# Optimization experiments

Measured on AMD Instinct MI355X. Metric: run time of the kernel, lower is better.

## Reference

```python
import jax, jax.numpy as jnp
import numpy as np

N = 13627
E = 504378
D = 500


def _seg_softmax(e, seg, n):
    m = jax.ops.segment_max(e, seg, num_segments=n)
    ex = jnp.exp(e - m[seg])
    s = jax.ops.segment_sum(ex, seg, num_segments=n)
    return ex / (s[seg] + 1e-16)


def _gatv2(x, src, dst, Wl, Wr, att, b, n):
    # PyG GATv2Conv (heads=1): message = Wl x_src; score uses Wl x_src + Wr x_dst
    xl = x @ Wl                                   # [N, F]
    xr = x @ Wr                                   # [N, F]
    e = jax.nn.leaky_relu(xl[src] + xr[dst], 0.2) @ att   # [E]
    a = _seg_softmax(e, dst, n)                   # segment softmax over targets
    out = jax.ops.segment_sum(a[:, None] * xl[src], dst, num_segments=n)
    return out + b


def setup_inputs() -> dict:
    key = jax.random.key(0)
    ks = jax.random.split(key, 24)
    s = 0.05
    inp = {
        'x': jax.random.normal(ks[0], (N, D), dtype=jnp.float32),
        'edge_index': jax.random.randint(ks[1], (2, E), 0, N),
        'neg_edge_index': jax.random.randint(ks[2], (2, E), 0, N),
        'Wl1': jax.random.normal(ks[3], (D, 300)) * s,
        'Wr1': jax.random.normal(ks[4], (D, 300)) * s,
        'att1': jax.random.normal(ks[5], (300,)) * s,
        'b1': jnp.zeros((300,)),
        'Wl2': jax.random.normal(ks[6], (300, 100)) * s,
        'Wr2': jax.random.normal(ks[7], (300, 100)) * s,
        'att2': jax.random.normal(ks[8], (100,)) * s,
        'b2': jnp.zeros((100,)),
        'Wl3': jax.random.normal(ks[9], (100, 1)) * s,
        'Wr3': jax.random.normal(ks[10], (100, 1)) * s,
        'att3': jax.random.normal(ks[11], (1,)) * s,
        'b3': jnp.zeros((1,)),
        'W_lin1': jax.random.normal(ks[12], (D, 100)) * s,
        'b_lin1': jnp.zeros((100,)),
        'W_lin2': jax.random.normal(ks[13], (D, 100)) * s,
        'b_lin2': jnp.zeros((100,)),
        'c1': jnp.array([0.5], dtype=jnp.float32),
        'c2': jnp.array([0.5], dtype=jnp.float32),
    }
    return inp


def reference(x, edge_index, neg_edge_index, Wl1, Wr1, att1, b1, Wl2, Wr2, att2, b2,
              Wl3, Wr3, att3, b3, W_lin1, b_lin1, W_lin2, b_lin2, c1, c2):
    # eval mode: dropout / dropout_adj are identity
    loops = jnp.arange(N)
    src = jnp.concatenate([edge_index[0], loops])   # GATv2Conv adds self loops
    dst = jnp.concatenate([edge_index[1], loops])

    h1 = jax.nn.relu(_gatv2(x, src, dst, Wl1, Wr1, att1, b1, N))
    h2 = jax.nn.relu(_gatv2(h1, src, dst, Wl2, Wr2, att2, b2, N))

    xo = h2 + jax.nn.relu(x @ W_lin1 + b_lin1)
    z = h2 + jax.nn.relu(x @ W_lin2 + b_lin2)

    # link-prediction reconstruction loss
    pos_s = jnp.sum(z[edge_index[0]] * z[edge_index[1]], axis=1)
    pos_loss = -jnp.mean(jnp.log(jax.nn.sigmoid(pos_s) + 1e-15))
    neg_s = jnp.sum(z[neg_edge_index[0]] * z[neg_edge_index[1]], axis=1)
    neg_loss = -jnp.mean(jnp.log(1.0 - jax.nn.sigmoid(neg_s) + 1e-15))
    r_loss = pos_loss + neg_loss

    out = _gatv2(xo, src, dst, Wl3, Wr3, att3, b3, N)   # [N, 1]
    return out, r_loss, c1, c2
```

## Files before the change

### kernel.cpp

```cpp
#include <hip/hip_runtime.h>
#include <hip/hip_bf16.h>

#define NODES 13627
#define DIM   500

typedef short short8 __attribute__((ext_vector_type(8)));
typedef float f32x4 __attribute__((ext_vector_type(4)));
typedef float floatx2 __attribute__((ext_vector_type(2)));

__device__ inline float wave_reduce_sum(float v) {
#pragma unroll
    for (int o = 32; o > 0; o >>= 1) v += __shfl_xor(v, o, 64);
    return v;
}

__device__ inline void store_v(float* p, float v) { *p = v; }
__device__ inline void store_v(__hip_bfloat16* p, float v) { *p = __float2bfloat16(v); }

__device__ inline float blo(unsigned w) { unsigned t = w << 16;        return __builtin_bit_cast(float, t); }
__device__ inline float bhi(unsigned w) { unsigned t = w & 0xffff0000u; return __builtin_bit_cast(float, t); }

__device__ inline unsigned char to_fp8(float v) {
    int r = __builtin_amdgcn_cvt_pk_fp8_f32(v, v, 0, false);
    return (unsigned char)(r & 0xff);
}

__device__ inline unsigned pk2bf(float a, float b) {
    unsigned la = (unsigned)__builtin_bit_cast(unsigned short, __float2bfloat16(a));
    unsigned hb = (unsigned)__builtin_bit_cast(unsigned short, __float2bfloat16(b));
    return la | (hb << 16);
}

template <int CTRL>
__device__ inline float dpp_add_step(float v) {
    int s = __builtin_amdgcn_update_dpp(0, __builtin_bit_cast(int, v), CTRL, 0xf, 0xf, true);
    return v + __builtin_bit_cast(float, s);
}
__device__ inline float quad16_reduce(float v) {
    v = dpp_add_step<0x128>(v);
    v = dpp_add_step<0x124>(v);
    v = dpp_add_step<0x4E>(v);
    v = dpp_add_step<0xB1>(v);
    return v;
}

struct b4 { __hip_bfloat16 a, b, c, d; };

__global__ __launch_bounds__(256) void hist_kernel(const int* __restrict__ dst,
                                                   int* __restrict__ cnt, int E) {
    int i = blockIdx.x * blockDim.x + threadIdx.x;
    if (i < E) atomicAdd(&cnt[dst[i]], 1);
}

__global__ __launch_bounds__(1024) void scan_kernel(int* __restrict__ cnt_cur,
                                                    int* __restrict__ off, int n) {
    __shared__ int wsum[16];
    const int tid = threadIdx.x, lane = tid & 63, w = tid >> 6;
    int carry = 0;
    for (int base = 0; base < n; base += 1024) {
        int i = base + tid;
        int v = (i < n) ? cnt_cur[i] : 0;
        int s = v;
#pragma unroll
        for (int o = 1; o < 64; o <<= 1) {
            int t = __shfl_up(s, o, 64);
            if (lane >= o) s += t;
        }
        if (lane == 63) wsum[w] = s;
        __syncthreads();
        if (w == 0 && lane < 16) {
            int x = wsum[lane];
            int sx = x;
#pragma unroll
            for (int o = 1; o < 16; o <<= 1) {
                int t = __shfl_up(sx, o, 64);
                if (lane >= o) sx += t;
            }
            wsum[lane] = sx;
        }
        __syncthreads();
        int wo = (w == 0) ? 0 : wsum[w - 1];
        int total = wsum[15];
        int excl = carry + wo + (s - v);
        if (i < n) { off[i] = excl; cnt_cur[i] = excl; }
        carry += total;
        __syncthreads();
    }
    if (tid == 0) off[n] = carry;
}

__global__ __launch_bounds__(256) void scatter_kernel(const int* __restrict__ src,
                                                      const int* __restrict__ dst,
                                                      int* __restrict__ cur,
                                                      int* __restrict__ ssrc, int E) {
    int i = blockIdx.x * blockDim.x + threadIdx.x;
    if (i < E) {
        int p = atomicAdd(&cur[dst[i]], 1);
        ssrc[p] = src[i];
    }
}

__global__ __launch_bounds__(256) void convert_all_kernel(
    const float* __restrict__ x,
    const float* __restrict__ Wl1, const float* __restrict__ Wr1,
    const float* __restrict__ Wl2, const float* __restrict__ Wr2,
    const float* __restrict__ Ws1, const float* __restrict__ Ws2,
    const float* __restrict__ bs1, const float* __restrict__ bs2,
    __hip_bfloat16* __restrict__ W1T, __hip_bfloat16* __restrict__ W2T,
    __hip_bfloat16* __restrict__ WsT, float* __restrict__ bcat,
    __hip_bfloat16* __restrict__ xb, int M) {
    int i = blockIdx.x * 256 + threadIdx.x;
    if (i < 327680) {
        int n = i >> 9, k = i & 511;
        float v = 0.f;
        if (k < 500) {
            if (n < 300) v = Wl1[k * 300 + n];
            else if (n < 600) v = Wr1[k * 300 + n - 300];
        }
        W1T[i] = __float2bfloat16(v);
    } else if (i < 409600) {
        int j = i - 327680;
        int n = j / 320, k = j - n * 320;
        float v = 0.f;
        if (k < 300) {
            if (n < 100) v = Wl2[k * 100 + n];
            else if (n < 200) v = Wr2[k * 100 + n - 100];
        }
        W2T[j] = __float2bfloat16(v);
    } else if (i < 540672) {
        int j = i - 409600;
        int n = j >> 9, k = j & 511;
        float v = 0.f;
        if (k < 500) {
            if (n < 100) v = Ws1[k * 100 + n];
            else if (n < 200) v = Ws2[k * 100 + n - 100];
        }
        WsT[j] = __float2bfloat16(v);
    } else if (i < 540928) {
        int n = i - 540672;
        float v = 0.f;
        if (n < 100) v = bs1[n];
        else if (n < 200) v = bs2[n - 100];
        bcat[n] = v;
    } else {
        int j = i - 540928;
        if (j >= M * 128) return;
        int m = j >> 7, k = (j & 127) << 2;
        b4 o;
        if (k < 500) {
            float4 v = *(const float4*)(x + (size_t)m * 500 + k);
            o.a = __float2bfloat16(v.x); o.b = __float2bfloat16(v.y);
            o.c = __float2bfloat16(v.z); o.d = __float2bfloat16(v.w);
        } else {
            o.a = o.b = o.c = o.d = __float2bfloat16(0.f);
        }
        *(b4*)(xb + (size_t)m * 512 + k) = o;
    }
}

template <int EPI, typename TC>
__global__ __launch_bounds__(256) void mfma_gemm(
    const __hip_bfloat16* __restrict__ A, const __hip_bfloat16* __restrict__ BT,
    TC* __restrict__ C, const float* __restrict__ bias, const float* __restrict__ h2,
    unsigned char* __restrict__ p8, __hip_bfloat16* __restrict__ pb,
    int M, int Kp, int Nn, int ldc) {
    __shared__ short AsF[8 * 64 * 8];
    __shared__ short BsF[4 * 64 * 8];
    const int t = threadIdx.x;
    const int w = t >> 6, lane = t & 63;
    const int c = t & 3, rr = t >> 2;
    const int m0 = blockIdx.y * 128, n0 = blockIdx.x * 64;

    f32x4 acc[2][4];
#pragma unroll
    for (int i = 0; i < 2; i++)
#pragma unroll
        for (int j = 0; j < 4; j++) acc[i][j] = (f32x4){0.f, 0.f, 0.f, 0.f};

    for (int k0 = 0; k0 < Kp; k0 += 32) {
#pragma unroll
        for (int r = 0; r < 2; r++) {
            int m = r * 64 + rr;
            int gm = m0 + m; if (gm >= M) gm = M - 1;
            float4 v = *(const float4*)(A + (size_t)gm * Kp + k0 + c * 8);
            int mi = m >> 4, sl = m & 15;
            *(float4*)(&AsF[(mi * 64 + c * 16 + sl) * 8]) = v;
        }
        {
            int n = rr;
            float4 v = *(const float4*)(BT + (size_t)(n0 + n) * Kp + k0 + c * 8);
            int ni = n >> 4, sl = n & 15;
            *(float4*)(&BsF[(ni * 64 + c * 16 + sl) * 8]) = v;
        }
        __syncthreads();
        short8 a0 = *(const short8*)(&AsF[((w * 2 + 0) * 64 + lane) * 8]);
        short8 a1 = *(const short8*)(&AsF[((w * 2 + 1) * 64 + lane) * 8]);
#pragma unroll
        for (int j = 0; j < 4; j++) {
            short8 b = *(const short8*)(&BsF[(j * 64 + lane) * 8]);
            acc[0][j] = __builtin_amdgcn_mfma_f32_16x16x32_bf16(a0, b, acc[0][j], 0, 0, 0);
            acc[1][j] = __builtin_amdgcn_mfma_f32_16x16x32_bf16(a1, b, acc[1][j], 0, 0, 0);
        }
        __syncthreads();
    }

    const int q = lane >> 4, sl = lane & 15;
#pragma unroll
    for (int i = 0; i < 2; i++) {
#pragma unroll
        for (int j = 0; j < 4; j++) {
#pragma unroll
            for (int reg = 0; reg < 4; reg++) {
                int gm = m0 + w * 32 + i * 16 + q * 4 + reg;
                int gn = n0 + j * 16 + sl;
                if (gm >= M) continue;
                float v = acc[i][j][reg];
                if constexpr (EPI == 1) {
                    if (gn < 300)       p8[(size_t)gm * 304 + gn] = to_fp8(v);
                    else if (gn < 600)  pb[(size_t)gm * 320 + (gn - 300)] = __float2bfloat16(v);
                    else if (gn < 620)  pb[(size_t)gm * 320 + (gn - 300)] = __float2bfloat16(0.f);
                    else if (gn < 624)  p8[(size_t)gm * 304 + (gn - 320)] = 0;
                } else if constexpr (EPI == 2) {
                    if (gn < 100)       p8[(size_t)gm * 112 + gn] = to_fp8(v);
                    else if (gn < 200)  pb[(size_t)gm * 128 + (gn - 100)] = __float2bfloat16(v);
                    else if (gn < 212)  p8[(size_t)gm * 112 + (gn - 100)] = 0;
                    else if (gn < 240)  pb[(size_t)gm * 128 + (gn - 112)] = __float2bfloat16(0.f);
                } else if constexpr (EPI == 3) {
                    if (gn < 200) {
                        int cn = gn < 100 ? gn : gn - 100;
                        float val = fmaxf(v + bias[gn], 0.f) + h2[(size_t)gm * 100 + cn];
                        if (gn < 100) C[(size_t)gm * 100 + gn] = val;
                        else p8[(size_t)gm * 128 + (gn - 100)] = to_fp8(val);
                    } else if (gn < 228) {
                        p8[(size_t)gm * 128 + (gn - 100)] = 0;
                    }
                } else {
                    store_v(&C[(size_t)gm * ldc + gn], v);
                }
            }
        }
    }
}

template <int F, int NJ, int SL8, int SRB, int SOUT, int JSL, typename TOUT>
__global__ __launch_bounds__(64, 4) void gat_f8_kernel(
    const unsigned char* __restrict__ xl8, const __hip_bfloat16* __restrict__ xrb,
    const float* __restrict__ att, const float* __restrict__ bias,
    const int* __restrict__ off, const int* __restrict__ ssrc,
    TOUT* __restrict__ out, int n) {
    const int lane = threadIdx.x;
    const int sl = lane & 15, q = lane >> 4;
    const int wid = blockIdx.x;

    floatx2 attv[NJ * 2], xrv[NJ * 2], acc[NJ * 2];
    const unsigned* xru = (const unsigned*)xrb + (size_t)wid * (SRB / 2);
#pragma unroll
    for (int j = 0; j < NJ; j++) {
        const int f0 = sl * 4 + j * 64;
        if (f0 < F) {
            float4 a4 = *(const float4*)(att + f0);
            attv[j * 2 + 0] = (floatx2){a4.x, a4.y};
            attv[j * 2 + 1] = (floatx2){a4.z, a4.w};
        } else {
            attv[j * 2 + 0] = (floatx2){0.f, 0.f};
            attv[j * 2 + 1] = (floatx2){0.f, 0.f};
        }
        unsigned u0 = __builtin_nontemporal_load(xru + (f0 >> 1));
        unsigned u1 = __builtin_nontemporal_load(xru + (f0 >> 1) + 1);
        xrv[j * 2 + 0] = (floatx2){blo(u0), bhi(u0)};
        xrv[j * 2 + 1] = (floatx2){blo(u1), bhi(u1)};
        acc[j * 2 + 0] = (floatx2){0.f, 0.f};
        acc[j * 2 + 1] = (floatx2){0.f, 0.f};
    }

    const int s0 = off[wid], s1 = off[wid + 1];
    const int eb = s0 - 1;
    const int ee = s1;
    float den = 0.f;
    const int myoff = sl * 4;

    int srcB;
    unsigned u[NJ];
    {
        int eq0 = eb + q;
        int srcA = wid;
        if (eq0 >= s0 && eq0 < ee) srcA = __builtin_nontemporal_load(ssrc + eq0);
        int eq1 = eb + 4 + q;
        srcB = wid;
        if (eq1 >= s0 && eq1 < ee) srcB = __builtin_nontemporal_load(ssrc + eq1);
        const unsigned char* row = xl8 + (size_t)srcA * SL8;
#pragma unroll
        for (int j = 0; j < NJ; j++) {
            const bool ld = (j < NJ - 1) || (sl < JSL);
            u[j] = ld ? *(const unsigned*)(row + myoff + j * 64) : 0u;
        }
    }

    float p_pend = 0.f, gate = 0.f;
    unsigned u_pend[NJ];
#pragma unroll
    for (int j = 0; j < NJ; j++) u_pend[j] = 0u;

    for (int e0 = eb; e0 < ee; e0 += 4) {
        int srcC = wid;
        {
            int eq2 = e0 + 8 + q;
            if (eq2 >= s0 && eq2 < ee) srcC = __builtin_nontemporal_load(ssrc + eq2);
        }
        unsigned un[NJ];
        {
            const unsigned char* row1 = xl8 + (size_t)srcB * SL8;
#pragma unroll
            for (int j = 0; j < NJ; j++) {
                const bool ld = (j < NJ - 1) || (sl < JSL);
                un[j] = ld ? *(const unsigned*)(row1 + myoff + j * 64) : 0u;
            }
        }
        {
            float pp = quad16_reduce(p_pend);
            float ex = gate * __expf(pp);
            den += ex;
            floatx2 ex2 = (floatx2){ex, ex};
#pragma unroll
            for (int j = 0; j < NJ; j++) {
                floatx2 lo = __builtin_amdgcn_cvt_pk_f32_fp8((int)u_pend[j], false);
                floatx2 hi = __builtin_amdgcn_cvt_pk_f32_fp8((int)u_pend[j], true);
                acc[j * 2 + 0] += ex2 * lo;
                acc[j * 2 + 1] += ex2 * hi;
            }
        }
        {
            floatx2 p2 = (floatx2){0.f, 0.f};
#pragma unroll
            for (int j = 0; j < NJ; j++) {
                floatx2 lo = __builtin_amdgcn_cvt_pk_f32_fp8((int)u[j], false);
                floatx2 hi = __builtin_amdgcn_cvt_pk_f32_fp8((int)u[j], true);
                floatx2 s0v = lo + xrv[j * 2 + 0];
                floatx2 s1v = hi + xrv[j * 2 + 1];
                floatx2 g0 = __builtin_elementwise_max(s0v, 0.2f * s0v);
                floatx2 g1 = __builtin_elementwise_max(s1v, 0.2f * s1v);
                p2 += attv[j * 2 + 0] * g0;
                p2 += attv[j * 2 + 1] * g1;
            }
            p_pend = p2.x + p2.y;
            gate = ((e0 + q) < ee) ? 1.f : 0.f;
        }
#pragma unroll
        for (int j = 0; j < NJ; j++) { u_pend[j] = u[j]; u[j] = un[j]; }
        srcB = srcC;
    }
    {
        float pp = quad16_reduce(p_pend);
        float ex = gate * __expf(pp);
        den += ex;
        floatx2 ex2 = (floatx2){ex, ex};
#pragma unroll
        for (int j = 0; j < NJ; j++) {
            floatx2 lo = __builtin_amdgcn_cvt_pk_f32_fp8((int)u_pend[j], false);
            floatx2 hi = __builtin_amdgcn_cvt_pk_f32_fp8((int)u_pend[j], true);
            acc[j * 2 + 0] += ex2 * lo;
            acc[j * 2 + 1] += ex2 * hi;
        }
    }

    float* af = (float*)acc;
#pragma unroll
    for (int o = 16; o <= 32; o <<= 1) {
        den += __shfl_xor(den, o, 64);
#pragma unroll
        for (int i = 0; i < NJ * 4; i++) af[i] += __shfl_xor(af[i], o, 64);
    }

    if (q == 0) {
        const float inv = 1.f / (den + 1e-16f);
#pragma unroll
        for (int j = 0; j < NJ; j++) {
            const int f0 = sl * 4 + j * 64;
            if (f0 >= SOUT) continue;
            float r[4];
#pragma unroll
            for (int cc = 0; cc < 4; cc++) {
                const int f = f0 + cc;
                float v = 0.f;
                if (f < F) v = fmaxf(af[j * 4 + cc] * inv + bias[f], 0.f);
                r[cc] = v;
            }
            if constexpr (sizeof(TOUT) == 4) {
                *(float4*)((float*)out + (size_t)wid * SOUT + f0) =
                    make_float4(r[0], r[1], r[2], r[3]);
            } else {
                unsigned* op = (unsigned*)out + (size_t)wid * (SOUT / 2) + (f0 >> 1);
                op[0] = pk2bf(r[0], r[1]);
                op[1] = pk2bf(r[2], r[3]);
            }
        }
    }
}

__global__ __launch_bounds__(256) void gemm_vec1_kernel(
    const float* __restrict__ xo, const float* __restrict__ wl,
    const float* __restrict__ wr, float* __restrict__ xl3,
    float* __restrict__ xr3, int M, int ldx) {
    const int wid = blockIdx.x * 4 + (threadIdx.x >> 6);
    const int lane = threadIdx.x & 63;
    if (wid >= M) return;
    float a = 0.f, b = 0.f;
    for (int f = lane; f < 100; f += 64) {
        float v = xo[(size_t)wid * ldx + f];
        a += v * wl[f];
        b += v * wr[f];
    }
    a = wave_reduce_sum(a);
    b = wave_reduce_sum(b);
    if (lane == 0) { xl3[wid] = a; xr3[wid] = b; }
}

__global__ __launch_bounds__(256) void gat3_kernel(
    const float* __restrict__ xl3, const float* __restrict__ xr3,
    const float* __restrict__ att3, const float* __restrict__ b3,
    const int* __restrict__ off, const int* __restrict__ ssrc,
    float* __restrict__ out, int n) {
    const int wid = blockIdx.x * 4 + (threadIdx.x >> 6);
    const int lane = threadIdx.x & 63;
    if (wid >= n) return;
    const float xrv = xr3[wid];
    const float att = att3[0];
    float num = 0.f, den = 0.f;
    const int s0 = off[wid], s1 = off[wid + 1];
    for (int e = s0 - 1 + lane; e < s1; e += 64) {
        int src = (e < s0) ? wid : ssrc[e];
        float xlv = xl3[src];
        float t = xlv + xrv;
        float g = t > 0.f ? t : 0.2f * t;
        float ex = __expf(g * att);
        den += ex;
        num += ex * xlv;
    }
    num = wave_reduce_sum(num);
    den = wave_reduce_sum(den);
    if (lane == 0) out[wid] = num / (den + 1e-16f) + b3[0];
}

__global__ __launch_bounds__(256) void loss_kernel(
    const unsigned char* __restrict__ z8, const int* __restrict__ pos,
    const int* __restrict__ neg, float* __restrict__ part, int nb, int E) {
    const int lane = threadIdx.x & 63;
    const int sl = lane & 15;
    const int wlocal = threadIdx.x >> 6;
    const int q = lane >> 4;
    const int nq = gridDim.x * 16;
    const int qid = (blockIdx.x * 4 + wlocal) * 4 + q;
    const int total = 2 * E;
    float psum = 0.f, nsum = 0.f;

    for (int base = qid; base < total; base += 4 * nq) {
        uint2 au[4], bu[4];
        bool act[4], isN[4];
#pragma unroll
        for (int s = 0; s < 4; s++) {
            int it = base + s * nq;
            act[s] = it < total;
            int itc = act[s] ? it : 0;
            isN[s] = itc >= E;
            int e = isN[s] ? itc - E : itc;
            const int* ei = isN[s] ? neg : pos;
            int u = ei[e], v = ei[E + e];
            au[s] = *(const uint2*)(z8 + (size_t)u * 128 + sl * 8);
            bu[s] = *(const uint2*)(z8 + (size_t)v * 128 + sl * 8);
        }
#pragma unroll
        for (int s = 0; s < 4; s++) {
            floatx2 a0 = __builtin_amdgcn_cvt_pk_f32_fp8((int)au[s].x, false);
            floatx2 a1 = __builtin_amdgcn_cvt_pk_f32_fp8((int)au[s].x, true);
            floatx2 a2 = __builtin_amdgcn_cvt_pk_f32_fp8((int)au[s].y, false);
            floatx2 a3 = __builtin_amdgcn_cvt_pk_f32_fp8((int)au[s].y, true);
            floatx2 b0 = __builtin_amdgcn_cvt_pk_f32_fp8((int)bu[s].x, false);
            floatx2 b1 = __builtin_amdgcn_cvt_pk_f32_fp8((int)bu[s].x, true);
            floatx2 b2 = __builtin_amdgcn_cvt_pk_f32_fp8((int)bu[s].y, false);
            floatx2 b3 = __builtin_amdgcn_cvt_pk_f32_fp8((int)bu[s].y, true);
            float p = a0.x * b0.x + a0.y * b0.y + a1.x * b1.x + a1.y * b1.y
                    + a2.x * b2.x + a2.y * b2.y + a3.x * b3.x + a3.y * b3.y;
            p = quad16_reduce(p);
            if (sl == 0 && act[s]) {
                float sig = __builtin_amdgcn_rcpf(1.f + __expf(-p));
                if (isN[s]) nsum += __logf(1.f - sig + 1e-15f);
                else        psum += __logf(sig + 1e-15f);
            }
        }
    }
    float pw = wave_reduce_sum(psum);
    float nw = wave_reduce_sum(nsum);
    __shared__ float sp[4], sn[4];
    if (lane == 0) { sp[wlocal] = pw; sn[wlocal] = nw; }
    __syncthreads();
    if (threadIdx.x == 0) {
        part[blockIdx.x]      = sp[0] + sp[1] + sp[2] + sp[3];
        part[nb + blockIdx.x] = sn[0] + sn[1] + sn[2] + sn[3];
    }
}

__global__ __launch_bounds__(1024) void finalize_kernel(
    const float* __restrict__ part, int nb,
    const float* __restrict__ c1, const float* __restrict__ c2,
    float* __restrict__ out, int n, int E) {
    __shared__ float sp[16], sn[16];
    const int tid = threadIdx.x, lane = tid & 63, w = tid >> 6;
    float p = 0.f, q = 0.f;
    for (int i = tid; i < nb; i += 1024) { p += part[i]; q += part[nb + i]; }
    p = wave_reduce_sum(p);
    q = wave_reduce_sum(q);
    if (lane == 0) { sp[w] = p; sn[w] = q; }
    __syncthreads();
    if (tid == 0) {
        float tp = 0.f, tq = 0.f;
#pragma unroll
        for (int i = 0; i < 16; i++) { tp += sp[i]; tq += sn[i]; }
        out[n]     = -(tp + tq) / (float)E;
        out[n + 1] = c1[0];
        out[n + 2] = c2[0];
    }
}

extern "C" void kernel_launch(void* const* d_in, const int* in_sizes, int n_in,
                              void* d_out, int out_size, void* d_ws, size_t ws_size,
                              hipStream_t stream) {
    const float* x      = (const float*)d_in[0];
    const int*   ei     = (const int*)d_in[1];
    const int*   nei    = (const int*)d_in[2];
    const float* Wl1    = (const float*)d_in[3];
    const float* Wr1    = (const float*)d_in[4];
    const float* att1   = (const float*)d_in[5];
    const float* b1     = (const float*)d_in[6];
    const float* Wl2    = (const float*)d_in[7];
    const float* Wr2    = (const float*)d_in[8];
    const float* att2   = (const float*)d_in[9];
    const float* b2     = (const float*)d_in[10];
    const float* Wl3    = (const float*)d_in[11];
    const float* Wr3    = (const float*)d_in[12];
    const float* att3   = (const float*)d_in[13];
    const float* b3     = (const float*)d_in[14];
    const float* Wlin1  = (const float*)d_in[15];
    const float* blin1  = (const float*)d_in[16];
    const float* Wlin2  = (const float*)d_in[17];
    const float* blin2  = (const float*)d_in[18];
    const float* c1     = (const float*)d_in[19];
    const float* c2     = (const float*)d_in[20];
    float* out = (float*)d_out;

    const int E = in_sizes[1] / 2;
    const int N = NODES;
    const int LOSS_BLOCKS = 4096;

    char* ws = (char*)d_ws;
    unsigned char*  xl8  = (unsigned char*)(ws + 0);
    unsigned char*  xl28 = (unsigned char*)(ws + 0);
    __hip_bfloat16* xrb  = (__hip_bfloat16*)(ws + 4194304);
    __hip_bfloat16* xr2b = (__hip_bfloat16*)(ws + 4194304);
    float*          xo   = (float*)(ws + 4194304);
    unsigned char*  z8   = (unsigned char*)(ws + 9645312);
    __hip_bfloat16* h1b  = (__hip_bfloat16*)(ws + 12915712);
    float*          h2   = (float*)(ws + 12915712);
    __hip_bfloat16* xb   = (__hip_bfloat16*)(ws + 21637120);
    __hip_bfloat16* W1T  = (__hip_bfloat16*)(ws + 35591168);
    __hip_bfloat16* W2T  = (__hip_bfloat16*)(ws + 36246528);
    __hip_bfloat16* WsT  = (__hip_bfloat16*)(ws + 36410368);
    float*          bcat = (float*)(ws + 36672512);
    float*          xl3  = (float*)(ws + 36673536);
    float*          xr3  = (float*)(ws + 36728064);
    int*            ioff = (int*)(ws + 36782592);
    int*            cur  = (int*)(ws + 36837376);
    int*            ssrc = (int*)(ws + 36892160);
    float*          part = (float*)(ws + 38909952);

    hipMemsetAsync(cur, 0, sizeof(int) * N, stream);

    hist_kernel<<<(E + 255) / 256, 256, 0, stream>>>(ei + E, cur, E);
    scan_kernel<<<1, 1024, 0, stream>>>(cur, ioff, N);
    scatter_kernel<<<(E + 255) / 256, 256, 0, stream>>>(ei, ei + E, cur, ssrc, E);

    convert_all_kernel<<<(540928 + N * 128 + 255) / 256, 256, 0, stream>>>(
        x, Wl1, Wr1, Wl2, Wr2, Wlin1, Wlin2, blin1, blin2,
        W1T, W2T, WsT, bcat, xb, N);

    mfma_gemm<1, __hip_bfloat16><<<dim3(10, 107), 256, 0, stream>>>(
        xb, W1T, (__hip_bfloat16*)nullptr, nullptr, nullptr, xl8, xrb, N, 512, 640, 0);
    gat_f8_kernel<300, 5, 304, 320, 320, 11, __hip_bfloat16>
        <<<N, 64, 0, stream>>>(xl8, xrb, att1, b1, ioff, ssrc, h1b, N);

    mfma_gemm<2, __hip_bfloat16><<<dim3(4, 107), 256, 0, stream>>>(
        h1b, W2T, (__hip_bfloat16*)nullptr, nullptr, nullptr, xl28, xr2b, N, 320, 256, 0);
    gat_f8_kernel<100, 2, 112, 128, 100, 9, float>
        <<<N, 64, 0, stream>>>(xl28, xr2b, att2, b2, ioff, ssrc, h2, N);

    mfma_gemm<3, float><<<dim3(4, 107), 256, 0, stream>>>(
        xb, WsT, xo, bcat, h2, z8, nullptr, N, 512, 256, 0);

    loss_kernel<<<LOSS_BLOCKS, 256, 0, stream>>>(z8, ei, nei, part, LOSS_BLOCKS, E);

    gemm_vec1_kernel<<<(N + 3) / 4, 256, 0, stream>>>(xo, Wl3, Wr3, xl3, xr3, N, 100);
    gat3_kernel<<<(N + 3) / 4, 256, 0, stream>>>(xl3, xr3, att3, b3, ioff, ssrc, out, N);

    finalize_kernel<<<1, 1024, 0, stream>>>(part, LOSS_BLOCKS, c1, c2, out, N, E);
}
```

Baseline: 356.1 us.

## Fuse skip-linear GEMM into layer-1 GEMM and histogram into convert kernel

Concatenates the two skip-linear weight matrices with the layer-1 GAT weights so one GEMM of width 896 computes both. The ReLU+bias skip pre-activation goes to a float scratch buffer, and a small elementwise kernel later adds h2 and writes xo and the fp8 z. The edge histogram atomics are also folded into the convert kernel, which removes one launch. The cost is an extra float round-trip of the skip pre-activation through memory and a wider first GEMM grid.

```diff
diff --git a/kernel.cpp b/kernel.cpp
--- a/kernel.cpp
+++ b/kernel.cpp
@@ -45,12 +45,6 @@
 }
 
 struct b4 { __hip_bfloat16 a, b, c, d; };
-
-__global__ __launch_bounds__(256) void hist_kernel(const int* __restrict__ dst,
-                                                   int* __restrict__ cnt, int E) {
-    int i = blockIdx.x * blockDim.x + threadIdx.x;
-    if (i < E) atomicAdd(&cnt[dst[i]], 1);
-}
 
 __global__ __launch_bounds__(1024) void scan_kernel(int* __restrict__ cnt_cur,
                                                     int* __restrict__ off, int n) {
@@ -106,10 +100,11 @@
     const float* __restrict__ Wl2, const float* __restrict__ Wr2,
     const float* __restrict__ Ws1, const float* __restrict__ Ws2,
     const float* __restrict__ bs1, const float* __restrict__ bs2,
-    __hip_bfloat16* __restrict__ W1T, __hip_bfloat16* __restrict__ W2T,
-    __hip_bfloat16* __restrict__ WsT, float* __restrict__ bcat,
-    __hip_bfloat16* __restrict__ xb, int M) {
+    __hip_bfloat16* __restrict__ WcT, __hip_bfloat16* __restrict__ W2T,
+    float* __restrict__ bcat, __hip_bfloat16* __restrict__ xb,
+    const int* __restrict__ dst, int* __restrict__ cnt, int E, int M) {
     int i = blockIdx.x * 256 + threadIdx.x;
+    if (i < E) atomicAdd(&cnt[dst[i]], 1);
     if (i < 327680) {
         int n = i >> 9, k = i & 511;
         float v = 0.f;
@@ -117,7 +112,7 @@
             if (n < 300) v = Wl1[k * 300 + n];
             else if (n < 600) v = Wr1[k * 300 + n - 300];
         }
-        W1T[i] = __float2bfloat16(v);
+        WcT[i] = __float2bfloat16(v);
     } else if (i < 409600) {
         int j = i - 327680;
         int n = j / 320, k = j - n * 320;
@@ -135,7 +130,7 @@
             if (n < 100) v = Ws1[k * 100 + n];
             else if (n < 200) v = Ws2[k * 100 + n - 100];
         }
-        WsT[j] = __float2bfloat16(v);
+        WcT[327680 + j] = __float2bfloat16(v);
     } else if (i < 540928) {
         int n = i - 540672;
         float v = 0.f;
@@ -220,25 +215,35 @@
                     else if (gn < 600)  pb[(size_t)gm * 320 + (gn - 300)] = __float2bfloat16(v);
                     else if (gn < 620)  pb[(size_t)gm * 320 + (gn - 300)] = __float2bfloat16(0.f);
                     else if (gn < 624)  p8[(size_t)gm * 304 + (gn - 320)] = 0;
+                    else if (gn >= 640 && gn < 840) {
+                        int cn = gn - 640;
+                        ((float*)C)[(size_t)gm * 200 + cn] = fmaxf(v + bias[cn], 0.f);
+                    }
                 } else if constexpr (EPI == 2) {
                     if (gn < 100)       p8[(size_t)gm * 112 + gn] = to_fp8(v);
                     else if (gn < 200)  pb[(size_t)gm * 128 + (gn - 100)] = __float2bfloat16(v);
                     else if (gn < 212)  p8[(size_t)gm * 112 + (gn - 100)] = 0;
                     else if (gn < 240)  pb[(size_t)gm * 128 + (gn - 112)] = __float2bfloat16(0.f);
-                } else if constexpr (EPI == 3) {
-                    if (gn < 200) {
-                        int cn = gn < 100 ? gn : gn - 100;
-                        float val = fmaxf(v + bias[gn], 0.f) + h2[(size_t)gm * 100 + cn];
-                        if (gn < 100) C[(size_t)gm * 100 + gn] = val;
-                        else p8[(size_t)gm * 128 + (gn - 100)] = to_fp8(val);
-                    } else if (gn < 228) {
-                        p8[(size_t)gm * 128 + (gn - 100)] = 0;
-                    }
                 } else {
                     store_v(&C[(size_t)gm * ldc + gn], v);
                 }
             }
         }
+    }
+}
+
+__global__ __launch_bounds__(256) void skip_add_kernel(
+    const float* __restrict__ pre, const float* __restrict__ h2,
+    float* __restrict__ xo, unsigned char* __restrict__ z8, int n) {
+    int tid = blockIdx.x * 256 + threadIdx.x;
+    if (tid >= n * 128) return;
+    int m = tid >> 7, k = tid & 127;
+    if (k < 100) {
+        float h = h2[(size_t)m * 100 + k];
+        xo[(size_t)m * 100 + k] = pre[(size_t)m * 200 + k] + h;
+        z8[(size_t)m * 128 + k] = to_fp8(pre[(size_t)m * 200 + 100 + k] + h);
+    } else {
+        z8[(size_t)m * 128 + k] = 0;
     }
 }
 
@@ -561,9 +566,8 @@
     __hip_bfloat16* h1b  = (__hip_bfloat16*)(ws + 12915712);
     float*          h2   = (float*)(ws + 12915712);
     __hip_bfloat16* xb   = (__hip_bfloat16*)(ws + 21637120);
-    __hip_bfloat16* W1T  = (__hip_bfloat16*)(ws + 35591168);
-    __hip_bfloat16* W2T  = (__hip_bfloat16*)(ws + 36246528);
-    __hip_bfloat16* WsT  = (__hip_bfloat16*)(ws + 36410368);
+    __hip_bfloat16* WcT  = (__hip_bfloat16*)(ws + 35591168);
+    __hip_bfloat16* W2T  = (__hip_bfloat16*)(ws + 36508672);
     float*          bcat = (float*)(ws + 36672512);
     float*          xl3  = (float*)(ws + 36673536);
     float*          xr3  = (float*)(ws + 36728064);
@@ -571,19 +575,19 @@
     int*            cur  = (int*)(ws + 36837376);
     int*            ssrc = (int*)(ws + 36892160);
     float*          part = (float*)(ws + 38909952);
+    float*          wpre = (float*)(ws + 39000064);
 
     hipMemsetAsync(cur, 0, sizeof(int) * N, stream);
 
-    hist_kernel<<<(E + 255) / 256, 256, 0, stream>>>(ei + E, cur, E);
+    convert_all_kernel<<<(540928 + N * 128 + 255) / 256, 256, 0, stream>>>(
+        x, Wl1, Wr1, Wl2, Wr2, Wlin1, Wlin2, blin1, blin2,
+        WcT, W2T, bcat, xb, ei + E, cur, E, N);
+
     scan_kernel<<<1, 1024, 0, stream>>>(cur, ioff, N);
     scatter_kernel<<<(E + 255) / 256, 256, 0, stream>>>(ei, ei + E, cur, ssrc, E);
 
-    convert_all_kernel<<<(540928 + N * 128 + 255) / 256, 256, 0, stream>>>(
-        x, Wl1, Wr1, Wl2, Wr2, Wlin1, Wlin2, blin1, blin2,
-        W1T, W2T, WsT, bcat, xb, N);
-
-    mfma_gemm<1, __hip_bfloat16><<<dim3(10, 107), 256, 0, stream>>>(
-        xb, W1T, (__hip_bfloat16*)nullptr, nullptr, nullptr, xl8, xrb, N, 512, 640, 0);
+    mfma_gemm<1, float><<<dim3(14, 107), 256, 0, stream>>>(
+        xb, WcT, wpre, bcat, nullptr, xl8, xrb, N, 512, 896, 200);
     gat_f8_kernel<300, 5, 304, 320, 320, 11, __hip_bfloat16>
         <<<N, 64, 0, stream>>>(xl8, xrb, att1, b1, ioff, ssrc, h1b, N);
 
@@ -592,8 +596,7 @@
     gat_f8_kernel<100, 2, 112, 128, 100, 9, float>
         <<<N, 64, 0, stream>>>(xl28, xr2b, att2, b2, ioff, ssrc, h2, N);
 
-    mfma_gemm<3, float><<<dim3(4, 107), 256, 0, stream>>>(
-        xb, WsT, xo, bcat, h2, z8, nullptr, N, 512, 256, 0);
+    skip_add_kernel<<<(N * 128 + 255) / 256, 256, 0, stream>>>(wpre, h2, xo, z8, N);
 
     loss_kernel<<<LOSS_BLOCKS, 256, 0, stream>>>(z8, ei, nei, part, LOSS_BLOCKS, E);
 
```

Result: faster. 341.2 us (-4.2%).
